# Performance work log

Measured on AMD Instinct MI355X. Metric: run time of the kernel, lower is better.

The kernel has to match this reference:

```python
import jax, jax.numpy as jnp
import numpy as np

EMB = 1024
HEADS = 16
HEAD_DIM = EMB // HEADS
ROPE_BASE = 10000.0


def rotate_half(x):
    # Interleaved rotate: pairs (x0,x1,x2,x3,...) -> (-x1,x0,-x3,x2,...)
    x1 = x[..., ::2]
    x2 = x[..., 1::2]
    return jnp.stack((-x2, x1), axis=-1).reshape(x.shape)


def rope_cos_sin(seq_len, head_dim):
    inv_freq = 1.0 / (ROPE_BASE ** (jnp.arange(0, head_dim, 2, dtype=jnp.float32) / head_dim))
    pos = jnp.arange(seq_len, dtype=jnp.float32)
    freqs = jnp.outer(pos, inv_freq)            # [S, hd/2]
    emb = jnp.concatenate([freqs, freqs], -1)   # [S, hd]  (NOTE: concat, matching source)
    return jnp.cos(emb)[None, None], jnp.sin(emb)[None, None]  # [1,1,S,hd]


def setup_inputs() -> dict:
    key = jax.random.key(0)
    ks = jax.random.split(key, 5)
    B, S = 2, 2048
    x = jax.random.normal(ks[0], (B, S, EMB), dtype=jnp.float32)
    scale = EMB ** -0.5
    Wq = jax.random.normal(ks[1], (EMB, EMB), dtype=jnp.float32) * scale
    Wk = jax.random.normal(ks[2], (EMB, EMB), dtype=jnp.float32) * scale
    Wv = jax.random.normal(ks[3], (EMB, EMB), dtype=jnp.float32) * scale
    Wo = jax.random.normal(ks[4], (EMB, EMB), dtype=jnp.float32) * scale
    return {"x": x, "Wq": Wq, "Wk": Wk, "Wv": Wv, "Wo": Wo}


def reference(x, Wq, Wk, Wv, Wo):
    B, S, E = x.shape
    def shape_heads(t):
        return t.reshape(B, S, HEADS, HEAD_DIM).transpose(0, 2, 1, 3)  # [B,H,S,hd]
    q = shape_heads(x @ Wq.T)
    k = shape_heads(x @ Wk.T)
    v = shape_heads(x @ Wv.T)
    cos, sin = rope_cos_sin(S, HEAD_DIM)
    q = q * cos + rotate_half(q) * sin
    k = k * cos + rotate_half(k) * sin
    scale = HEAD_DIM ** -0.5
    scores = jnp.einsum('bhqd,bhkd->bhqk', q, k) * scale  # [B,H,S,S]
    causal = jnp.triu(jnp.ones((S, S), dtype=bool), k=1)
    scores = jnp.where(causal, -jnp.inf, scores)
    attn = jax.nn.softmax(scores, axis=-1)
    out = jnp.einsum('bhqk,bhkd->bhqd', attn, v)           # [B,H,S,hd]
    out = out.transpose(0, 2, 1, 3).reshape(B, S, E)
    return out @ Wo.T
```

## Files before the change

kernel.cpp:

```cpp
#include <hip/hip_runtime.h>
#include <cstdint>
#include <cstddef>

typedef __bf16 bf16;
typedef __attribute__((ext_vector_type(8))) __bf16 bf16x8;
typedef __attribute__((ext_vector_type(4))) __bf16 bf16x4;
typedef __attribute__((ext_vector_type(4))) float f32x4;

constexpr int kS = 2048;
constexpr int kH = 16;
constexpr int kD = 64;

__device__ __forceinline__ void gload16(const bf16* g, bf16* l) {
  __builtin_amdgcn_global_load_lds((const __attribute__((address_space(1))) void*)g,
                                   (__attribute__((address_space(3))) void*)l, 16, 0, 0);
}

__global__ __launch_bounds__(256) void cast_all_kernel(
    const float* __restrict__ x, const float* __restrict__ wq, const float* __restrict__ wk,
    const float* __restrict__ wv, const float* __restrict__ wo,
    bf16* __restrict__ xb, bf16* __restrict__ wqb, bf16* __restrict__ wkb,
    bf16* __restrict__ wvb, bf16* __restrict__ wob) {
  int idx = blockIdx.x * 256 + threadIdx.x;
  const float* src; bf16* dst; int i;
  if (idx < (1 << 19)) { src = x; dst = xb; i = idx << 3; }
  else {
    int r = idx - (1 << 19);
    int t = r >> 17;
    i = (r & ((1 << 17) - 1)) << 3;
    src = (t == 0) ? wq : (t == 1) ? wk : (t == 2) ? wv : wo;
    dst = (t == 0) ? wqb : (t == 1) ? wkb : (t == 2) ? wvb : wob;
  }
  float4 v0 = *(const float4*)(src + i);
  float4 v1 = *(const float4*)(src + i + 4);
  bf16x8 o;
  o[0] = (bf16)v0.x; o[1] = (bf16)v0.y; o[2] = (bf16)v0.z; o[3] = (bf16)v0.w;
  o[4] = (bf16)v1.x; o[5] = (bf16)v1.y; o[6] = (bf16)v1.z; o[7] = (bf16)v1.w;
  *(bf16x8*)(dst + i) = o;
}


#define GSTAGE(BUF, KT)                                    \
  gload16(aP0 + (KT), &As[BUF][(w * 64 + l) * 8]);         \
  gload16(aP1 + (KT), &As[BUF][((4 + w) * 64 + l) * 8]);   \
  gload16(bP0 + (KT), &Bs[BUF][(w * 64 + l) * 8]);         \
  gload16(bP1 + (KT), &Bs[BUF][((4 + w) * 64 + l) * 8]);

__global__ __launch_bounds__(256) void gemm_qkv(const bf16* __restrict__ A,
                                                const bf16* __restrict__ wq,
                                                const bf16* __restrict__ wk,
                                                const bf16* __restrict__ wv,
                                                bf16* __restrict__ qo,
                                                bf16* __restrict__ ko,
                                                bf16* __restrict__ vto) {
  __shared__ bf16 As[2][128 * 32];
  __shared__ bf16 Bs[2][128 * 32];
  const int tid = threadIdx.x;
  const int w = tid >> 6, l = tid & 63;
  const int wr = w >> 1, wc = w & 1;
  const int lr = l & 15, lg = l >> 4;

  const int xcd = blockIdx.x & 7;
  const int idx = blockIdx.x >> 3;
  const int which = idx >> 5;
  const int rem = idx & 31;
  const int mblk = ((xcd >> 1) << 3) + (rem >> 2);
  const int npanel = ((xcd & 1) << 2) + (rem & 3);
  const int m0 = mblk * 128;
  const int n0 = npanel * 128;
  const bf16* Bw = (which == 0) ? wq : (which == 1) ? wk : wv;

  const int srow = l >> 2;
  const int skcol = ((l & 3) ^ ((l >> 3) & 3)) << 3;
  const int K = 1024;

  const bf16* aP0 = A + (size_t)(m0 + w * 16 + srow) * K + skcol;
  const bf16* aP1 = A + (size_t)(m0 + 64 + w * 16 + srow) * K + skcol;
  const bf16* bP0 = Bw + (size_t)(n0 + w * 16 + srow) * K + skcol;
  const bf16* bP1 = Bw + (size_t)(n0 + 64 + w * 16 + srow) * K + skcol;

  f32x4 acc[4][4] = {};
  const int ca = (lg ^ ((lr >> 1) & 3)) * 8;

  GSTAGE(0, 0)
  __syncthreads();
  int cur = 0;
  for (int kt = 0; kt < K; kt += 32) {
    if (kt + 32 < K) { GSTAGE(cur ^ 1, kt + 32) }
    bf16x8 af[4], bfg[4];
#pragma unroll
    for (int mi = 0; mi < 4; mi++)
      af[mi] = *(const bf16x8*)&As[cur][(wr * 64 + mi * 16 + lr) * 32 + ca];
#pragma unroll
    for (int ni = 0; ni < 4; ni++)
      bfg[ni] = *(const bf16x8*)&Bs[cur][(wc * 64 + ni * 16 + lr) * 32 + ca];
    __builtin_amdgcn_s_setprio(1);
#pragma unroll
    for (int mi = 0; mi < 4; mi++)
#pragma unroll
      for (int ni = 0; ni < 4; ni++)
        acc[mi][ni] = __builtin_amdgcn_mfma_f32_16x16x32_bf16(af[mi], bfg[ni], acc[mi][ni], 0, 0, 0);
    __builtin_amdgcn_s_setprio(0);
    __syncthreads();
    cur ^= 1;
  }

  float invf_[4];
#pragma unroll
  for (int ni = 0; ni < 4; ni++) {
    int d31 = ((n0 + wc * 64 + ni * 16 + lr) & 63) & 31;
    invf_[ni] = exp2f((float)d31 * -0.41524100480466348f);
  }

#pragma unroll
  for (int mi = 0; mi < 4; mi++) {
#pragma unroll
    for (int ni = 0; ni < 4; ni++) {
#pragma unroll
      for (int r = 0; r < 4; r++) {
        const int m = m0 + wr * 64 + mi * 16 + lg * 4 + r;
        const int n = n0 + wc * 64 + ni * 16 + lr;
        float v = acc[mi][ni][r];
        const int st = m & 2047;
        const size_t bh = (size_t)(m >> 11) * kH + (n >> 6);
        if (which < 2) {
          float vp = __shfl_xor(v, 1);
          const int d = n & 63;
          float th = (float)st * invf_[ni];
          float sth = __sinf(th), cth = __cosf(th);
          float rv = v * cth + ((d & 1) ? vp : -vp) * sth;
          if (which == 1) rv *= 0.18033688011112042f;
          bf16* dst = which ? ko : qo;
          dst[((bh << 11) + st) * kD + d] = (bf16)rv;
        } else {
          int pos = (st & ~31) | (((st >> 2) & 3) << 3) | (((st >> 4) & 1) << 2) | (st & 3);
          vto[((bh * kD + (n & 63)) << 11) + pos] = (bf16)v;
        }
      }
    }
  }
}

__global__ __launch_bounds__(256) void gemm_out(const bf16* __restrict__ A,
                                                const bf16* __restrict__ Bw,
                                                float* __restrict__ Cout) {
  __shared__ bf16 As[2][64 * 32];
  __shared__ bf16 Bs[2][128 * 32];
  const int tid = threadIdx.x;
  const int w = tid >> 6, l = tid & 63;
  const int wr = w >> 1, wc = w & 1;
  const int lr = l & 15, lg = l >> 4;
  const int bid = blockIdx.x;
  const int xcd = bid & 7;
  const int r5 = bid >> 3;
  const int m0 = (((xcd << 3) + (r5 >> 3))) * 64;
  const int n0 = (r5 & 7) * 128;
  const int K = 1024, N = 1024;

  const int srow = l >> 2;
  const int skcol = ((l & 3) ^ ((l >> 3) & 3)) << 3;

  const bf16* aP0 = A + (size_t)(m0 + w * 16 + srow) * K + skcol;
  const bf16* bP0 = Bw + (size_t)(n0 + w * 16 + srow) * K + skcol;
  const bf16* bP1 = Bw + (size_t)(n0 + 64 + w * 16 + srow) * K + skcol;

  f32x4 acc[2][4] = {};
  const int ca = (lg ^ ((lr >> 1) & 3)) * 8;

#define OSTAGE(BUF, KT)                                    \
  gload16(aP0 + (KT), &As[BUF][(w * 64 + l) * 8]);         \
  gload16(bP0 + (KT), &Bs[BUF][(w * 64 + l) * 8]);         \
  gload16(bP1 + (KT), &Bs[BUF][((4 + w) * 64 + l) * 8]);

  OSTAGE(0, 0)
  __syncthreads();
  int cur = 0;
  for (int kt = 0; kt < K; kt += 32) {
    if (kt + 32 < K) { OSTAGE(cur ^ 1, kt + 32) }
    bf16x8 af[2], bfg[4];
#pragma unroll
    for (int mi = 0; mi < 2; mi++)
      af[mi] = *(const bf16x8*)&As[cur][(wr * 32 + mi * 16 + lr) * 32 + ca];
#pragma unroll
    for (int ni = 0; ni < 4; ni++)
      bfg[ni] = *(const bf16x8*)&Bs[cur][(wc * 64 + ni * 16 + lr) * 32 + ca];
    __builtin_amdgcn_s_setprio(1);
#pragma unroll
    for (int mi = 0; mi < 2; mi++)
#pragma unroll
      for (int ni = 0; ni < 4; ni++)
        acc[mi][ni] = __builtin_amdgcn_mfma_f32_16x16x32_bf16(af[mi], bfg[ni], acc[mi][ni], 0, 0, 0);
    __builtin_amdgcn_s_setprio(0);
    __syncthreads();
    cur ^= 1;
  }
#undef OSTAGE

#pragma unroll
  for (int mi = 0; mi < 2; mi++)
#pragma unroll
    for (int ni = 0; ni < 4; ni++)
#pragma unroll
      for (int r = 0; r < 4; r++) {
        const int m = m0 + wr * 32 + mi * 16 + lg * 4 + r;
        const int n = n0 + wc * 64 + ni * 16 + lr;
        Cout[(size_t)m * N + n] = acc[mi][ni][r];
      }
}

#define STAGE(BUF, KV0)                                                                  \
  {                                                                                      \
    _Pragma("unroll") for (int j_ = 0; j_ < 4; j_++) {                                   \
      const int ch_ = w * 4 + j_;                                                        \
      gload16(kh + (size_t)((KV0) + (ch_ >> 1) * 16 + lr) * 64 + (ch_ & 1) * 32 + lg * 8, \
              &Ks[BUF][ch_ * 512 + l * 8]);                                              \
    }                                                                                    \
    _Pragma("unroll") for (int j_ = 0; j_ < 4; j_++) {                                   \
      const int ch_ = w * 4 + j_;                                                        \
      gload16(vh + (size_t)((ch_ >> 2) * 16 + lr) * 2048 + (KV0) + (ch_ & 3) * 32 + lg * 8, \
              &Vs[BUF][ch_ * 512 + l * 8]);                                              \
    }                                                                                    \
  }

#define COMPUTE(BUF, DIAG, O, LPART, QF, QROW, KVB)                                      \
  {                                                                                      \
    bf16x8 kf_[8][2];                                                                    \
    _Pragma("unroll") for (int s_ = 0; s_ < 8; s_++)                                     \
      _Pragma("unroll") for (int c_ = 0; c_ < 2; c_++)                                   \
        kf_[s_][c_] = *(const bf16x8*)&Ks[BUF][(s_ * 2 + c_) * 512 + l * 8];             \
    f32x4 sa_[8] = {};                                                                   \
    __builtin_amdgcn_s_setprio(1);                                                       \
    _Pragma("unroll") for (int s_ = 0; s_ < 8; s_++) {                                   \
      sa_[s_] = __builtin_amdgcn_mfma_f32_16x16x32_bf16(kf_[s_][0], QF[0], sa_[s_], 0, 0, 0); \
      sa_[s_] = __builtin_amdgcn_mfma_f32_16x16x32_bf16(kf_[s_][1], QF[1], sa_[s_], 0, 0, 0); \
    }                                                                                    \
    __builtin_amdgcn_s_setprio(0);                                                       \
    bf16x8 pf_[4];                                                                       \
    float sum0_ = 0.0f, sum1_ = 0.0f;                                                    \
    _Pragma("unroll") for (int s_ = 0; s_ < 8; s_++)                                     \
      _Pragma("unroll") for (int r_ = 0; r_ < 4; r_++) {                                 \
        float sc_ = sa_[s_][r_];                                                         \
        if (DIAG) {                                                                      \
          int kk_ = (KVB) + s_ * 16 + lg * 4 + r_;                                       \
          sc_ = (kk_ <= (QROW)) ? sc_ : -1e30f;                                          \
        }                                                                                \
        float e_ = exp2f(sc_);                                                           \
        if (s_ & 1) sum1_ += e_; else sum0_ += e_;                                       \
        pf_[s_ >> 1][(s_ & 1) * 4 + r_] = (bf16)e_;                                      \
      }                                                                                  \
    LPART += sum0_ + sum1_;                                                              \
    bf16x8 vf_[4][4];                                                                    \
    _Pragma("unroll") for (int c_ = 0; c_ < 4; c_++)                                     \
      _Pragma("unroll") for (int f_ = 0; f_ < 4; f_++)                                   \
        vf_[c_][f_] = *(const bf16x8*)&Vs[BUF][(c_ * 4 + f_) * 512 + l * 8];             \
    __builtin_amdgcn_s_setprio(1);                                                       \
    _Pragma("unroll") for (int c_ = 0; c_ < 4; c_++)                                     \
      _Pragma("unroll") for (int f_ = 0; f_ < 4; f_++)                                   \
        O[c_] = __builtin_amdgcn_mfma_f32_16x16x32_bf16(vf_[c_][f_], pf_[f_], O[c_], 0, 0, 0); \
    __builtin_amdgcn_s_setprio(0);                                                       \
  }

#define EPILOG(O, LPART, Q0)                                                             \
  {                                                                                      \
    float lt_ = LPART;                                                                   \
    lt_ += __shfl_xor(lt_, 16);                                                          \
    lt_ += __shfl_xor(lt_, 32);                                                          \
    const float inv_ = 1.0f / lt_;                                                       \
    _Pragma("unroll") for (int c_ = 0; c_ < 4; c_++) {                                   \
      bf16x4 ov_;                                                                        \
      _Pragma("unroll") for (int r_ = 0; r_ < 4; r_++) ov_[r_] = (bf16)(O[c_][r_] * inv_); \
      size_t addr_ = ((size_t)(b * kS + (Q0) + lr)) * (kH * kD) + h * 64 + c_ * 16 + lg * 4; \
      *(bf16x4*)&ob[addr_] = ov_;                                                        \
    }                                                                                    \
  }

__global__ __launch_bounds__(256, 2) void attn_kernel(const bf16* __restrict__ qb,
                                                      const bf16* __restrict__ kb,
                                                      const bf16* __restrict__ vtb,
                                                      bf16* __restrict__ ob) {
  __shared__ bf16 Ks[2][8192];
  __shared__ bf16 Vs[2][8192];
  const int tid = threadIdx.x;
  const int w = tid >> 6, l = tid & 63;
  const int lr = l & 15, lg = l >> 4;
  const int bid = blockIdx.x;
  const int bh = bid & 31;
  const int qt = 31 - (bid >> 5);
  const bf16* qh = qb + (size_t)bh * (kS * kD);
  const bf16* kh = kb + (size_t)bh * (kS * kD);
  const bf16* vh = vtb + (size_t)bh * (kS * kD);
  const int b = bh >> 4, h = bh & 15;

  const int q0 = qt * 64 + w * 16;
  const int q = q0 + lr;
  bf16x8 qf[2];
#pragma unroll
  for (int c = 0; c < 2; c++)
    qf[c] = *(const bf16x8*)&qh[(size_t)(q0 + lr) * kD + c * 32 + lg * 8];

  float lpart = 0.0f;
  f32x4 o[4] = {};
  const int nkv = (qt + 2) >> 1;

  STAGE(0, 0)
  __syncthreads();
  int cur = 0;
  for (int t = 0; t < nkv; t++) {
    if (t + 1 < nkv) STAGE(cur ^ 1, (t + 1) * 128)
    COMPUTE(cur, (t == nkv - 1), o, lpart, qf, q, t * 128)
    __syncthreads();
    cur ^= 1;
  }
  EPILOG(o, lpart, q0)
}

extern "C" void kernel_launch(void* const* d_in, const int* in_sizes, int n_in,
                              void* d_out, int out_size, void* d_ws, size_t ws_size,
                              hipStream_t stream) {
  const float* x  = (const float*)d_in[0];
  const float* wq = (const float*)d_in[1];
  const float* wk = (const float*)d_in[2];
  const float* wv = (const float*)d_in[3];
  const float* wo = (const float*)d_in[4];

  bf16* xb  = (bf16*)d_ws;
  bf16* qb  = xb + (1 << 22);
  bf16* kb  = qb + (1 << 22);
  bf16* vtb = kb + (1 << 22);
  bf16* ab  = vtb + (1 << 22);
  bf16* wqb = ab + (1 << 22);
  bf16* wkb = wqb + (1 << 20);
  bf16* wvb = wkb + (1 << 20);
  bf16* wob = wvb + (1 << 20);

  cast_all_kernel<<<4096, 256, 0, stream>>>(x, wq, wk, wv, wo, xb, wqb, wkb, wvb, wob);
  gemm_qkv<<<768, 256, 0, stream>>>(xb, wqb, wkb, wvb, qb, kb, vtb);
  attn_kernel<<<1024, 256, 0, stream>>>(qb, kb, vtb, ab);
  gemm_out<<<512, 256, 0, stream>>>(ab, wob, (float*)d_out);
}
```

Baseline: 108.6 us.

## Rewrite attention with 32x32x16 MFMA, 128-row query tiles and swizzled LDS

Switches the attention kernel from 16x16x32 to 32x32x16 bf16 MFMA. Each wave now handles 32 query rows, so a block covers 128 queries and half as many blocks are launched. K and V are staged into LDS with an XOR swizzle to avoid bank conflicts, and the V-transpose permutation in the QKV GEMM changes to match the new P operand layout. Block ordering is changed to pair heavy and light causal tiles. The goal is higher MFMA efficiency and more K/V reuse per block, at the cost of more registers per wave and fewer blocks for load balance.

New measurement: 121.7 us. 12.1% more time.

```diff
diff --git a/kernel.cpp b/kernel.cpp
--- a/kernel.cpp
+++ b/kernel.cpp
@@ -6,6 +6,7 @@
 typedef __attribute__((ext_vector_type(8))) __bf16 bf16x8;
 typedef __attribute__((ext_vector_type(4))) __bf16 bf16x4;
 typedef __attribute__((ext_vector_type(4))) float f32x4;
+typedef __attribute__((ext_vector_type(16))) float f32x16;
 
 constexpr int kS = 2048;
 constexpr int kH = 16;
@@ -133,7 +134,7 @@
           bf16* dst = which ? ko : qo;
           dst[((bh << 11) + st) * kD + d] = (bf16)rv;
         } else {
-          int pos = (st & ~31) | (((st >> 2) & 3) << 3) | (((st >> 4) & 1) << 2) | (st & 3);
+          int pos = (st & ~12) | (((st >> 2) & 1) << 3) | (((st >> 3) & 1) << 2);
           vto[((bh * kD + (n & 63)) << 11) + pos] = (bf16)v;
         }
       }
@@ -208,69 +209,55 @@
       }
 }
 
+
 #define STAGE(BUF, KV0)                                                                  \
   {                                                                                      \
-    _Pragma("unroll") for (int j_ = 0; j_ < 4; j_++) {                                   \
-      const int ch_ = w * 4 + j_;                                                        \
-      gload16(kh + (size_t)((KV0) + (ch_ >> 1) * 16 + lr) * 64 + (ch_ & 1) * 32 + lg * 8, \
+    _Pragma("unroll") for (int i_ = 0; i_ < 4; i_++) {                                   \
+      const int ch_ = w * 4 + i_;                                                        \
+      gload16(kh + (size_t)((KV0) + ch_ * 8 + (l >> 3)) * 64 + (((l & 7) ^ (l >> 3)) * 8), \
               &Ks[BUF][ch_ * 512 + l * 8]);                                              \
     }                                                                                    \
-    _Pragma("unroll") for (int j_ = 0; j_ < 4; j_++) {                                   \
-      const int ch_ = w * 4 + j_;                                                        \
-      gload16(vh + (size_t)((ch_ >> 2) * 16 + lr) * 2048 + (KV0) + (ch_ & 3) * 32 + lg * 8, \
+    _Pragma("unroll") for (int i_ = 0; i_ < 4; i_++) {                                   \
+      const int ch_ = w * 4 + i_;                                                        \
+      gload16(vh + (size_t)(ch_ * 4 + (l >> 4)) * 2048 + (KV0) +                         \
+                  (((l & 15) ^ (((ch_ & 1) << 2) + (l >> 4))) * 8),                      \
               &Vs[BUF][ch_ * 512 + l * 8]);                                              \
     }                                                                                    \
   }
 
-#define COMPUTE(BUF, DIAG, O, LPART, QF, QROW, KVB)                                      \
+#define COMPUTE(BUF, DIAG, KVB)                                                          \
   {                                                                                      \
-    bf16x8 kf_[8][2];                                                                    \
-    _Pragma("unroll") for (int s_ = 0; s_ < 8; s_++)                                     \
-      _Pragma("unroll") for (int c_ = 0; c_ < 2; c_++)                                   \
-        kf_[s_][c_] = *(const bf16x8*)&Ks[BUF][(s_ * 2 + c_) * 512 + l * 8];             \
-    f32x4 sa_[8] = {};                                                                   \
+    f32x16 sa_[4] = {};                                                                  \
     __builtin_amdgcn_s_setprio(1);                                                       \
-    _Pragma("unroll") for (int s_ = 0; s_ < 8; s_++) {                                   \
-      sa_[s_] = __builtin_amdgcn_mfma_f32_16x16x32_bf16(kf_[s_][0], QF[0], sa_[s_], 0, 0, 0); \
-      sa_[s_] = __builtin_amdgcn_mfma_f32_16x16x32_bf16(kf_[s_][1], QF[1], sa_[s_], 0, 0, 0); \
-    }                                                                                    \
+    _Pragma("unroll") for (int kb_ = 0; kb_ < 4; kb_++)                                  \
+      _Pragma("unroll") for (int ks_ = 0; ks_ < 4; ks_++) {                              \
+        bf16x8 kf_ = *(const bf16x8*)&Ks[BUF][(kb_ * 32 + (l & 31)) * 64 +               \
+                                             (((ks_ * 2 + hh) ^ (l & 7)) * 8)];          \
+        sa_[kb_] = __builtin_amdgcn_mfma_f32_32x32x16_bf16(kf_, qf[ks_], sa_[kb_], 0, 0, 0); \
+      }                                                                                  \
     __builtin_amdgcn_s_setprio(0);                                                       \
-    bf16x8 pf_[4];                                                                       \
-    float sum0_ = 0.0f, sum1_ = 0.0f;                                                    \
-    _Pragma("unroll") for (int s_ = 0; s_ < 8; s_++)                                     \
-      _Pragma("unroll") for (int r_ = 0; r_ < 4; r_++) {                                 \
-        float sc_ = sa_[s_][r_];                                                         \
+    _Pragma("unroll") for (int kb_ = 0; kb_ < 4; kb_++) {                                \
+      bf16x8 pf_[2];                                                                     \
+      float s0_ = 0.0f, s1_ = 0.0f;                                                      \
+      _Pragma("unroll") for (int r_ = 0; r_ < 16; r_++) {                                \
+        float sc_ = sa_[kb_][r_];                                                        \
         if (DIAG) {                                                                      \
-          int kk_ = (KVB) + s_ * 16 + lg * 4 + r_;                                       \
-          sc_ = (kk_ <= (QROW)) ? sc_ : -1e30f;                                          \
+          int kv_ = (KVB) + kb_ * 32 + (r_ & 3) + 8 * (r_ >> 2) + 4 * hh;                \
+          sc_ = (kv_ <= qrow) ? sc_ : -1e30f;                                            \
         }                                                                                \
         float e_ = exp2f(sc_);                                                           \
-        if (s_ & 1) sum1_ += e_; else sum0_ += e_;                                       \
-        pf_[s_ >> 1][(s_ & 1) * 4 + r_] = (bf16)e_;                                      \
+        if (r_ & 1) s1_ += e_; else s0_ += e_;                                           \
+        pf_[r_ >> 3][r_ & 7] = (bf16)e_;                                                 \
       }                                                                                  \
-    LPART += sum0_ + sum1_;                                                              \
-    bf16x8 vf_[4][4];                                                                    \
-    _Pragma("unroll") for (int c_ = 0; c_ < 4; c_++)                                     \
-      _Pragma("unroll") for (int f_ = 0; f_ < 4; f_++)                                   \
-        vf_[c_][f_] = *(const bf16x8*)&Vs[BUF][(c_ * 4 + f_) * 512 + l * 8];             \
-    __builtin_amdgcn_s_setprio(1);                                                       \
-    _Pragma("unroll") for (int c_ = 0; c_ < 4; c_++)                                     \
-      _Pragma("unroll") for (int f_ = 0; f_ < 4; f_++)                                   \
-        O[c_] = __builtin_amdgcn_mfma_f32_16x16x32_bf16(vf_[c_][f_], pf_[f_], O[c_], 0, 0, 0); \
-    __builtin_amdgcn_s_setprio(0);                                                       \
-  }
-
-#define EPILOG(O, LPART, Q0)                                                             \
-  {                                                                                      \
-    float lt_ = LPART;                                                                   \
-    lt_ += __shfl_xor(lt_, 16);                                                          \
-    lt_ += __shfl_xor(lt_, 32);                                                          \
-    const float inv_ = 1.0f / lt_;                                                       \
-    _Pragma("unroll") for (int c_ = 0; c_ < 4; c_++) {                                   \
-      bf16x4 ov_;                                                                        \
-      _Pragma("unroll") for (int r_ = 0; r_ < 4; r_++) ov_[r_] = (bf16)(O[c_][r_] * inv_); \
-      size_t addr_ = ((size_t)(b * kS + (Q0) + lr)) * (kH * kD) + h * 64 + c_ * 16 + lg * 4; \
-      *(bf16x4*)&ob[addr_] = ov_;                                                        \
+      lpart += s0_ + s1_;                                                                \
+      __builtin_amdgcn_s_setprio(1);                                                     \
+      _Pragma("unroll") for (int db_ = 0; db_ < 2; db_++)                                \
+        _Pragma("unroll") for (int sg_ = 0; sg_ < 2; sg_++) {                            \
+          bf16x8 vf_ = *(const bf16x8*)&Vs[BUF][(db_ * 32 + (l & 31)) * 128 +            \
+                                               (((kb_ * 4 + sg_ * 2 + hh) ^ (l & 7)) * 8)]; \
+          o[db_] = __builtin_amdgcn_mfma_f32_32x32x16_bf16(vf_, pf_[sg_], o[db_], 0, 0, 0); \
+        }                                                                                \
+      __builtin_amdgcn_s_setprio(0);                                                     \
     }                                                                                    \
   }
 
@@ -282,36 +269,49 @@
   __shared__ bf16 Vs[2][8192];
   const int tid = threadIdx.x;
   const int w = tid >> 6, l = tid & 63;
-  const int lr = l & 15, lg = l >> 4;
+  const int hh = l >> 5;
   const int bid = blockIdx.x;
   const int bh = bid & 31;
-  const int qt = 31 - (bid >> 5);
+  const int t5 = bid >> 5;
+  const int qt = (t5 < 8) ? (15 - t5) : (t5 - 8);
   const bf16* qh = qb + (size_t)bh * (kS * kD);
   const bf16* kh = kb + (size_t)bh * (kS * kD);
   const bf16* vh = vtb + (size_t)bh * (kS * kD);
   const int b = bh >> 4, h = bh & 15;
 
-  const int q0 = qt * 64 + w * 16;
-  const int q = q0 + lr;
-  bf16x8 qf[2];
-#pragma unroll
-  for (int c = 0; c < 2; c++)
-    qf[c] = *(const bf16x8*)&qh[(size_t)(q0 + lr) * kD + c * 32 + lg * 8];
+  const int q0 = qt * 128 + w * 32;
+  const int qrow = q0 + (l & 31);
+  bf16x8 qf[4];
+#pragma unroll
+  for (int ks = 0; ks < 4; ks++)
+    qf[ks] = *(const bf16x8*)&qh[(size_t)qrow * kD + ks * 16 + hh * 8];
 
   float lpart = 0.0f;
-  f32x4 o[4] = {};
-  const int nkv = (qt + 2) >> 1;
+  f32x16 o[2] = {};
+  const int nkv = qt + 1;
 
   STAGE(0, 0)
   __syncthreads();
   int cur = 0;
   for (int t = 0; t < nkv; t++) {
     if (t + 1 < nkv) STAGE(cur ^ 1, (t + 1) * 128)
-    COMPUTE(cur, (t == nkv - 1), o, lpart, qf, q, t * 128)
+    COMPUTE(cur, (t == nkv - 1), t * 128)
     __syncthreads();
     cur ^= 1;
   }
-  EPILOG(o, lpart, q0)
+
+  float lt = lpart + __shfl_xor(lpart, 32);
+  const float inv = 1.0f / lt;
+#pragma unroll
+  for (int db = 0; db < 2; db++)
+#pragma unroll
+    for (int rq = 0; rq < 4; rq++) {
+      bf16x4 ov;
+#pragma unroll
+      for (int e = 0; e < 4; e++) ov[e] = (bf16)(o[db][rq * 4 + e] * inv);
+      const int d0 = db * 32 + rq * 8 + hh * 4;
+      *(bf16x4*)&ob[((size_t)(b * kS + qrow)) * (kH * kD) + h * 64 + d0] = ov;
+    }
 }
 
 extern "C" void kernel_launch(void* const* d_in, const int* in_sizes, int n_in,
@@ -335,6 +335,6 @@
 
   cast_all_kernel<<<4096, 256, 0, stream>>>(x, wq, wk, wv, wo, xb, wqb, wkb, wvb, wob);
   gemm_qkv<<<768, 256, 0, stream>>>(xb, wqb, wkb, wvb, qb, kb, vtb);
-  attn_kernel<<<1024, 256, 0, stream>>>(qb, kb, vtb, ab);
+  attn_kernel<<<512, 256, 0, stream>>>(qb, kb, vtb, ab);
   gemm_out<<<512, 256, 0, stream>>>(ab, wob, (float*)d_out);
 }
```
